# Kernel optimization log

Measured on AMD Instinct MI355X. Metric: run time of the kernel, lower is better.

The kernel has to match this reference:

```python
import jax, jax.numpy as jnp
import numpy as np

B, F, V, C = 2048, 2048, 50257, 50257


def setup_inputs() -> dict:
    key = jax.random.key(0)
    ks = jax.random.split(key, 16)
    s = 0.02  # init scale
    return {
        "X": jax.random.randint(ks[0], (B,), 0, V),
        "h": jax.random.normal(ks[1], (B, F), jnp.float32),
        "c": jax.random.normal(ks[2], (B, F), jnp.float32),
        "emb": jax.random.normal(ks[3], (V, F), jnp.float32) * s,
        "Wf": jax.random.normal(ks[4], (2 * F, F), jnp.float32) * s,
        "bf": jnp.zeros((F,), jnp.float32),
        "Wi": jax.random.normal(ks[5], (2 * F, F), jnp.float32) * s,
        "bi": jnp.zeros((F,), jnp.float32),
        "Wig": jax.random.normal(ks[6], (2 * F, F), jnp.float32) * s,
        "big": jnp.zeros((F,), jnp.float32),
        "Wog": jax.random.normal(ks[7], (2 * F, F), jnp.float32) * s,
        "bog": jnp.zeros((F,), jnp.float32),
        "Wcls": jax.random.normal(ks[8], (F, C), jnp.float32) * s,
        "bcls": jnp.zeros((C,), jnp.float32),
    }


def reference(X, h, c, emb, Wf, bf, Wi, bi, Wig, big, Wog, bog, Wcls, bcls):
    # Embedding lookup: [B] -> [B, F]
    x = emb[X]
    xh = jnp.concatenate([x, h], axis=-1)  # [B, 2F]
    # Fuse the four gate GEMMs into one [B,2F] @ [2F,4F] matmul.
    Wg = jnp.concatenate([Wf, Wig, Wog, Wi], axis=1)   # [2F, 4F]
    bg = jnp.concatenate([bf, big, bog, bi], axis=0)   # [4F]
    gates = xh @ Wg + bg                                # [B, 4F]
    f_pre, ig_pre, og_pre, g_pre = jnp.split(gates, 4, axis=-1)
    forget_gate = jax.nn.sigmoid(f_pre)
    input_gate = jax.nn.sigmoid(ig_pre)
    output_gate = jax.nn.sigmoid(og_pre)
    g = jnp.tanh(g_pre)
    c_new = forget_gate * c + input_gate * g
    h_new = output_gate * jnp.tanh(c_new)
    y = h_new @ Wcls + bcls  # [B, C]
    return (y, h_new, c_new)
```

## Files before the change

### kernel.cpp

```cpp
#include <hip/hip_runtime.h>
#include <hip/hip_bf16.h>

typedef __attribute__((ext_vector_type(4))) float f32x4;
typedef __attribute__((ext_vector_type(8))) short short8;
typedef __attribute__((ext_vector_type(8))) unsigned short ushort8;
typedef __attribute__((ext_vector_type(4))) unsigned short u16x4;
typedef float f4a __attribute__((ext_vector_type(4), aligned(4)));

__device__ __forceinline__ unsigned short f2bf(float f) {
  unsigned int u = __float_as_uint(f);
  u += 0x7fffu + ((u >> 16) & 1u);
  return (unsigned short)(u >> 16);
}

#define BARRIER do { asm volatile("" ::: "memory"); __builtin_amdgcn_s_barrier(); asm volatile("" ::: "memory"); } while(0)
#define LGKM0   do { asm volatile("s_waitcnt lgkmcnt(0)" ::: "memory"); __builtin_amdgcn_sched_barrier(0); } while(0)
#define VMW(n)  asm volatile("s_waitcnt vmcnt(" #n ")" ::: "memory")

__global__ __launch_bounds__(256) void k_build_xh(
    const int* __restrict__ X, const float* __restrict__ h,
    const float* __restrict__ emb, unsigned short* __restrict__ xh) {
  int b = blockIdx.x;
  int tid = threadIdx.x;
  int j0 = tid * 16;
  const float* src;
  if (j0 < 2048) {
    int xb = X[b];
    src = emb + (size_t)xb * 2048 + j0;
  } else {
    src = h + (size_t)b * 2048 + (j0 - 2048);
  }
  unsigned short* dst = xh + (size_t)b * 4096 + j0;
#pragma unroll
  for (int half = 0; half < 2; ++half) {
    float4 f0 = *(const float4*)(src + half * 8);
    float4 f1 = *(const float4*)(src + half * 8 + 4);
    ushort8 o;
    o[0] = f2bf(f0.x); o[1] = f2bf(f0.y); o[2] = f2bf(f0.z); o[3] = f2bf(f0.w);
    o[4] = f2bf(f1.x); o[5] = f2bf(f1.y); o[6] = f2bf(f1.z); o[7] = f2bf(f1.w);
    *(ushort8*)(dst + half * 8) = o;
  }
}

__global__ __launch_bounds__(256) void k_cvt_t(
    const float* __restrict__ W, unsigned short* __restrict__ WT,
    int K, int Nin, int ldo, int rowoff) {
  int tid = threadIdx.x;
  int lane = tid & 63, w = tid >> 6;
  int n0 = blockIdx.x * 64, k0 = blockIdx.y * 64;
  int nb = n0 + 4 * (lane & 15);
  int kb = k0 + w * 16 + 4 * (lane >> 4);
  float v[4][4];
  if (nb + 3 < Nin) {
#pragma unroll
    for (int r = 0; r < 4; ++r) {
      f4a x = *(const f4a*)(W + (size_t)(kb + r) * Nin + nb);
      v[r][0] = x.x; v[r][1] = x.y; v[r][2] = x.z; v[r][3] = x.w;
    }
  } else {
#pragma unroll
    for (int r = 0; r < 4; ++r)
#pragma unroll
      for (int e = 0; e < 4; ++e)
        v[r][e] = (nb + e < Nin) ? W[(size_t)(kb + r) * Nin + nb + e] : 0.f;
  }
#pragma unroll
  for (int e = 0; e < 4; ++e) {
    if (nb + e < Nin) {
      u16x4 o;
      o[0] = f2bf(v[0][e]); o[1] = f2bf(v[1][e]);
      o[2] = f2bf(v[2][e]); o[3] = f2bf(v[3][e]);
      *(u16x4*)(WT + (size_t)(rowoff + nb + e) * ldo + kb) = o;
    }
  }
}

__device__ __forceinline__ void stage_unit(
    const unsigned short* __restrict__ gp0, int ld, int row0, int rowmax,
    int ktile, unsigned char* smem, unsigned lds_off, int tid, int wid) {
#pragma unroll
  for (int i = 0; i < 2; ++i) {
    unsigned phys = (unsigned)(i * 512 + tid) * 16u;
    unsigned logi = phys ^ (((phys >> 7) & 7u) << 4);
    int r = (int)(logi >> 7);
    int kb = (int)(logi & 127u);
    int grow = row0 + r;
    grow = (grow > rowmax) ? rowmax : grow;
    const unsigned short* gp = gp0 + (size_t)grow * ld + ktile * 64 + (kb >> 1);
    __builtin_amdgcn_global_load_lds(
        (const __attribute__((address_space(1))) void*)gp,
        (__attribute__((address_space(3))) void*)(smem + lds_off + (unsigned)(i * 512 + wid * 64) * 16u),
        16, 0, 0);
  }
}

__device__ __forceinline__ short8 ld_fragA(const unsigned char* smem, int buf, int half,
                                           int row_local, int ks, int lane) {
  unsigned kbyte = (unsigned)(ks * 64 + ((lane >> 4) << 4));
  unsigned off = (unsigned)(buf * 2 + half) * 16384u + (unsigned)row_local * 128u
               + (kbyte ^ (((unsigned)row_local & 7u) << 4));
  return *(const short8*)(smem + off);
}
__device__ __forceinline__ short8 ld_fragB(const unsigned char* smem, int buf, int half,
                                           int col_local, int ks, int lane) {
  unsigned kbyte = (unsigned)(ks * 64 + ((lane >> 4) << 4));
  unsigned off = 65536u + (unsigned)(buf * 2 + half) * 16384u + (unsigned)col_local * 128u
               + (kbyte ^ (((unsigned)col_local & 7u) << 4));
  return *(const short8*)(smem + off);
}

__global__ __launch_bounds__(512, 1) void k_gemm256(
    const unsigned short* __restrict__ A, const unsigned short* __restrict__ Bt,
    const float* __restrict__ bias, float* __restrict__ C,
    int N, int K, int lda, int ldb, int rowmaxB) {
  __shared__ __align__(16) unsigned char smem[131072];
  const int tid = threadIdx.x, lane = tid & 63, wid = tid >> 6;
  const int wr = wid >> 2, wc = wid & 3;

  int nwg = gridDim.x * gridDim.y;
  int o = blockIdx.y * gridDim.x + blockIdx.x;
  int q = nwg >> 3;
  int s = (o & 7) * q + (o >> 3);
  const int mrow0 = (s & 7) * 256;
  const int ncol0 = (s >> 3) * 256;

  const int NKT = K >> 6;

  f32x4 acc[8][4];
#pragma unroll
  for (int m = 0; m < 8; ++m)
#pragma unroll
    for (int n = 0; n < 4; ++n) acc[m][n] = {0.f, 0.f, 0.f, 0.f};

  short8 a_frag[4][2], b_frag[2][2][2];

#define ST_A(buf, h, t) stage_unit(A, lda, mrow0 + (h) * 128, 0x7fffffff, (t), smem, (unsigned)((buf) * 2 + (h)) * 16384u, tid, wid)
#define ST_B(buf, h, t) stage_unit(Bt, ldb, ncol0 + (h) * 128, rowmaxB, (t), smem, 65536u + (unsigned)((buf) * 2 + (h)) * 16384u, tid, wid)
#define RD_A(buf, mh) do { _Pragma("unroll") for (int mm = 0; mm < 4; ++mm) { int rl = (mh) * 64 + mm * 16 + (lane & 15); _Pragma("unroll") for (int ks = 0; ks < 2; ++ks) a_frag[mm][ks] = ld_fragA(smem, (buf), wr, rl, ks, lane); } } while (0)
#define RD_B(buf, nh) do { _Pragma("unroll") for (int nn = 0; nn < 2; ++nn) { int cl = (wc & 1) * 64 + (nh) * 32 + nn * 16 + (lane & 15); _Pragma("unroll") for (int ks = 0; ks < 2; ++ks) b_frag[nh][nn][ks] = ld_fragB(smem, (buf), (wc >> 1), cl, ks, lane); } } while (0)
#define MF(mh, nh) do { __builtin_amdgcn_s_setprio(1); _Pragma("unroll") for (int mm = 0; mm < 4; ++mm) _Pragma("unroll") for (int nn = 0; nn < 2; ++nn) _Pragma("unroll") for (int ks = 0; ks < 2; ++ks) acc[(mh) * 4 + mm][(nh) * 2 + nn] = __builtin_amdgcn_mfma_f32_16x16x32_bf16(a_frag[mm][ks], b_frag[(nh)][nn][ks], acc[(mh) * 4 + mm][(nh) * 2 + nn], 0, 0, 0); __builtin_amdgcn_s_setprio(0); } while (0)

  ST_A(0, 0, 0); ST_A(0, 1, 0); ST_B(0, 0, 0); ST_B(0, 1, 0);
  ST_B(1, 0, 1); ST_B(1, 1, 1);
  VMW(4); BARRIER;

  for (int t0 = 0; t0 + 3 < NKT; t0 += 2) {
    RD_A(0, 0); RD_B(0, 0); ST_A(1, 0, t0 + 1);
    BARRIER; LGKM0; MF(0, 0); BARRIER;
    RD_B(0, 1); ST_A(1, 1, t0 + 1);
    BARRIER; LGKM0; MF(0, 1); BARRIER;
    RD_A(0, 1); ST_B(0, 0, t0 + 2);
    BARRIER; LGKM0; MF(1, 1); BARRIER;
    ST_B(0, 1, t0 + 2); VMW(4);
    BARRIER; LGKM0; MF(1, 0); BARRIER;
    RD_A(1, 0); RD_B(1, 0); ST_A(0, 0, t0 + 2);
    BARRIER; LGKM0; MF(0, 0); BARRIER;
    RD_B(1, 1); ST_A(0, 1, t0 + 2);
    BARRIER; LGKM0; MF(0, 1); BARRIER;
    RD_A(1, 1); ST_B(1, 0, t0 + 3);
    BARRIER; LGKM0; MF(1, 1); BARRIER;
    ST_B(1, 1, t0 + 3); VMW(4);
    BARRIER; LGKM0; MF(1, 0); BARRIER;
  }

  {
    const int t1 = NKT - 1;
    RD_A(0, 0); RD_B(0, 0); ST_A(1, 0, t1);
    BARRIER; LGKM0; MF(0, 0); BARRIER;
    RD_B(0, 1); ST_A(1, 1, t1);
    BARRIER; LGKM0; MF(0, 1); BARRIER;
    RD_A(0, 1);
    BARRIER; LGKM0; MF(1, 1); BARRIER;
    VMW(0);
    BARRIER; LGKM0; MF(1, 0); BARRIER;
    RD_A(1, 0); RD_B(1, 0);
    BARRIER; LGKM0; MF(0, 0); BARRIER;
    RD_B(1, 1);
    BARRIER; LGKM0; MF(0, 1); BARRIER;
    RD_A(1, 1);
    BARRIER; LGKM0; MF(1, 1); BARRIER;
    BARRIER; LGKM0; MF(1, 0); BARRIER;
  }

  {
    float* wlds = (float*)(smem + (unsigned)wid * 16384u);
    const int gcol = ncol0 + wc * 64 + lane;
    const bool cok = (gcol < N);
    const float bv = (bias != nullptr && cok) ? bias[gcol] : 0.f;
#pragma unroll
    for (int mh = 0; mh < 2; ++mh) {
#pragma unroll
      for (int mm = 0; mm < 4; ++mm)
#pragma unroll
        for (int nn = 0; nn < 4; ++nn) {
#pragma unroll
          for (int r = 0; r < 4; ++r) {
            int row = mm * 16 + ((lane >> 4) << 2) + r;
            int colv = nn * 16 + (lane & 15);
            int cs = (colv + ((row >> 2) & 3) * 16) & 63;
            wlds[row * 64 + cs] = acc[mh * 4 + mm][nn][r];
          }
        }
#pragma unroll 8
      for (int row = 0; row < 64; ++row) {
        int cs = (lane + ((row >> 2) & 3) * 16) & 63;
        float v = wlds[row * 64 + cs] + bv;
        int grow = mrow0 + wr * 128 + mh * 64 + row;
        if (cok) C[(size_t)grow * N + gcol] = v;
      }
    }
  }
#undef ST_A
#undef ST_B
#undef RD_A
#undef RD_B
#undef MF
}

__global__ __launch_bounds__(256) void k_lstm(
    const float* __restrict__ gates, const float* __restrict__ c,
    const float* __restrict__ bfp, const float* __restrict__ bigp,
    const float* __restrict__ bogp, const float* __restrict__ bip,
    float* __restrict__ hnew, float* __restrict__ cnew,
    unsigned short* __restrict__ hnew_bf) {
  int idx = blockIdx.x * 256 + threadIdx.x;
  int b = idx >> 11, j = idx & 2047;
  const float* g = gates + (size_t)b * 8192;
  float fp  = g[j]        + bfp[j];
  float igp = g[2048 + j] + bigp[j];
  float ogp = g[4096 + j] + bogp[j];
  float gp  = g[6144 + j] + bip[j];
  float f  = 1.f / (1.f + expf(-fp));
  float ig = 1.f / (1.f + expf(-igp));
  float og = 1.f / (1.f + expf(-ogp));
  float gt = tanhf(gp);
  float cn = f * c[idx] + ig * gt;
  float hn = og * tanhf(cn);
  cnew[idx] = cn;
  hnew[idx] = hn;
  hnew_bf[idx] = f2bf(hn);
}

extern "C" void kernel_launch(void* const* d_in, const int* in_sizes, int n_in,
                              void* d_out, int out_size, void* d_ws, size_t ws_size,
                              hipStream_t stream) {
  const int B = 2048, F = 2048, C = 50257;
  const int NT = 50304;
  const int*   X    = (const int*)d_in[0];
  const float* h    = (const float*)d_in[1];
  const float* c    = (const float*)d_in[2];
  const float* emb  = (const float*)d_in[3];
  const float* Wf   = (const float*)d_in[4];
  const float* bf   = (const float*)d_in[5];
  const float* Wi   = (const float*)d_in[6];
  const float* bi   = (const float*)d_in[7];
  const float* Wig  = (const float*)d_in[8];
  const float* big  = (const float*)d_in[9];
  const float* Wog  = (const float*)d_in[10];
  const float* bog  = (const float*)d_in[11];
  const float* Wcls = (const float*)d_in[12];
  const float* bcls = (const float*)d_in[13];

  float* y    = (float*)d_out;
  float* hnew = y + (size_t)B * C;
  float* cnew = hnew + (size_t)B * F;

  char* ws = (char*)d_ws;
  unsigned short* hnbf  = (unsigned short*)ws;
  unsigned short* xh    = (unsigned short*)(ws + 8388608);
  unsigned short* WgT   = (unsigned short*)(ws + 25165824);
  float*          gates = (float*)(ws + 92274688);
  unsigned short* WclsT = (unsigned short*)(ws + 8388608);

  k_build_xh<<<B, 256, 0, stream>>>(X, h, emb, xh);

  const float* parts[4] = {Wf, Wig, Wog, Wi};
  for (int p = 0; p < 4; ++p)
    k_cvt_t<<<dim3(32, 64), 256, 0, stream>>>(parts[p], WgT, 4096, 2048, 4096, p * 2048);

  k_gemm256<<<dim3(8, 32), 512, 0, stream>>>(xh, WgT, nullptr, gates, 8192, 4096, 4096, 4096, 8191);

  k_lstm<<<(B * F) / 256, 256, 0, stream>>>(gates, c, bf, big, bog, bi,
                                            hnew, cnew, hnbf);

  k_cvt_t<<<dim3(786, 32), 256, 0, stream>>>(Wcls, WclsT, 2048, C, 2048, 0);

  k_gemm256<<<dim3(8, 197), 512, 0, stream>>>(hnbf, WclsT, bcls, y, C, 2048, 2048, 2048, NT - 1);
}
```

Measured before the change: 790.1 us.

## Fuse LSTM cell into gate GEMM epilogue, interleave gate weights, add classifier tail kernel

Gate weights are now transposed in a single launch and interleaved per 64-column group, so each 256-column gate GEMM tile holds all four gates for the same 64 hidden units. The LSTM nonlinearity and state update then run in the GEMM epilogue through LDS, which removes the fp32 gates buffer round trip and the separate k_lstm kernel. The classifier GEMM now covers 192 full 256-wide column tiles, and a new 128x128 tail kernel handles the remaining ~1100 columns so fewer clamped, wasted columns are computed. Staging addresses are precomputed once per kernel instead of recomputed each stage, and the sched_barrier after lgkmcnt waits is dropped, which may change instruction scheduling. The extra __syncthreads in the fused epilogue and the small, unpipelined tail kernel add some cost in exchange.

```diff
diff --git a/kernel.cpp b/kernel.cpp
--- a/kernel.cpp
+++ b/kernel.cpp
@@ -14,7 +14,7 @@
 }
 
 #define BARRIER do { asm volatile("" ::: "memory"); __builtin_amdgcn_s_barrier(); asm volatile("" ::: "memory"); } while(0)
-#define LGKM0   do { asm volatile("s_waitcnt lgkmcnt(0)" ::: "memory"); __builtin_amdgcn_sched_barrier(0); } while(0)
+#define LGKM    asm volatile("s_waitcnt lgkmcnt(0)" ::: "memory")
 #define VMW(n)  asm volatile("s_waitcnt vmcnt(" #n ")" ::: "memory")
 
 __global__ __launch_bounds__(256) void k_build_xh(
@@ -42,9 +42,36 @@
   }
 }
 
+__global__ __launch_bounds__(256) void k_cvt_wg(
+    const float* __restrict__ W0, const float* __restrict__ W1,
+    const float* __restrict__ W2, const float* __restrict__ W3,
+    unsigned short* __restrict__ WT) {
+  const int g = blockIdx.z;
+  const float* W = (g == 0) ? W0 : (g == 1) ? W1 : (g == 2) ? W2 : W3;
+  int tid = threadIdx.x, lane = tid & 63, w = tid >> 6;
+  int n0 = blockIdx.x * 64, k0 = blockIdx.y * 64;
+  int nb = n0 + 4 * (lane & 15);
+  int kb = k0 + w * 16 + 4 * (lane >> 4);
+  float v[4][4];
+#pragma unroll
+  for (int r = 0; r < 4; ++r) {
+    f4a x = *(const f4a*)(W + (size_t)(kb + r) * 2048 + nb);
+    v[r][0] = x.x; v[r][1] = x.y; v[r][2] = x.z; v[r][3] = x.w;
+  }
+#pragma unroll
+  for (int e = 0; e < 4; ++e) {
+    int col = nb + e;
+    int row = ((col >> 6) << 8) + g * 64 + (col & 63);
+    u16x4 o;
+    o[0] = f2bf(v[0][e]); o[1] = f2bf(v[1][e]);
+    o[2] = f2bf(v[2][e]); o[3] = f2bf(v[3][e]);
+    *(u16x4*)(WT + (size_t)row * 4096 + kb) = o;
+  }
+}
+
 __global__ __launch_bounds__(256) void k_cvt_t(
     const float* __restrict__ W, unsigned short* __restrict__ WT,
-    int K, int Nin, int ldo, int rowoff) {
+    int K, int Nin, int ldo) {
   int tid = threadIdx.x;
   int lane = tid & 63, w = tid >> 6;
   int n0 = blockIdx.x * 64, k0 = blockIdx.y * 64;
@@ -70,29 +97,16 @@
       u16x4 o;
       o[0] = f2bf(v[0][e]); o[1] = f2bf(v[1][e]);
       o[2] = f2bf(v[2][e]); o[3] = f2bf(v[3][e]);
-      *(u16x4*)(WT + (size_t)(rowoff + nb + e) * ldo + kb) = o;
-    }
-  }
-}
-
-__device__ __forceinline__ void stage_unit(
-    const unsigned short* __restrict__ gp0, int ld, int row0, int rowmax,
-    int ktile, unsigned char* smem, unsigned lds_off, int tid, int wid) {
-#pragma unroll
-  for (int i = 0; i < 2; ++i) {
-    unsigned phys = (unsigned)(i * 512 + tid) * 16u;
-    unsigned logi = phys ^ (((phys >> 7) & 7u) << 4);
-    int r = (int)(logi >> 7);
-    int kb = (int)(logi & 127u);
-    int grow = row0 + r;
-    grow = (grow > rowmax) ? rowmax : grow;
-    const unsigned short* gp = gp0 + (size_t)grow * ld + ktile * 64 + (kb >> 1);
-    __builtin_amdgcn_global_load_lds(
-        (const __attribute__((address_space(1))) void*)gp,
-        (__attribute__((address_space(3))) void*)(smem + lds_off + (unsigned)(i * 512 + wid * 64) * 16u),
-        16, 0, 0);
-  }
-}
+      *(u16x4*)(WT + (size_t)(nb + e) * ldo + kb) = o;
+    }
+  }
+}
+
+struct EpiP {
+  const float *c, *b0, *b1, *b2, *b3;
+  float *hnew, *cnew;
+  unsigned short* hnbf;
+};
 
 __device__ __forceinline__ short8 ld_fragA(const unsigned char* smem, int buf, int half,
                                            int row_local, int ks, int lane) {
@@ -109,10 +123,11 @@
   return *(const short8*)(smem + off);
 }
 
+template <int EPI>
 __global__ __launch_bounds__(512, 1) void k_gemm256(
     const unsigned short* __restrict__ A, const unsigned short* __restrict__ Bt,
     const float* __restrict__ bias, float* __restrict__ C,
-    int N, int K, int lda, int ldb, int rowmaxB) {
+    int N, int K, int lda, int ldb, int rowmaxB, EpiP P) {
   __shared__ __align__(16) unsigned char smem[131072];
   const int tid = threadIdx.x, lane = tid & 63, wid = tid >> 6;
   const int wr = wid >> 2, wc = wid & 3;
@@ -126,6 +141,24 @@
 
   const int NKT = K >> 6;
 
+  unsigned vA[2], vB[2][2];
+#pragma unroll
+  for (int i = 0; i < 2; ++i) {
+    unsigned phys = (unsigned)(i * 512 + tid) * 16u;
+    unsigned logi = phys ^ (((phys >> 7) & 7u) << 4);
+    unsigned r = logi >> 7;
+    unsigned kbe = (logi & 127u) >> 1;
+    vA[i] = r * (unsigned)lda + kbe;
+#pragma unroll
+    for (int hh = 0; hh < 2; ++hh) {
+      int br = ncol0 + hh * 128 + (int)r;
+      br = (br > rowmaxB) ? rowmaxB : br;
+      vB[hh][i] = (unsigned)br * (unsigned)ldb + kbe;
+    }
+  }
+  const unsigned short* Ab0 = A + (size_t)mrow0 * lda;
+  const unsigned short* Ab1 = Ab0 + (size_t)128 * lda;
+
   f32x4 acc[8][4];
 #pragma unroll
   for (int m = 0; m < 8; ++m)
@@ -134,8 +167,15 @@
 
   short8 a_frag[4][2], b_frag[2][2][2];
 
-#define ST_A(buf, h, t) stage_unit(A, lda, mrow0 + (h) * 128, 0x7fffffff, (t), smem, (unsigned)((buf) * 2 + (h)) * 16384u, tid, wid)
-#define ST_B(buf, h, t) stage_unit(Bt, ldb, ncol0 + (h) * 128, rowmaxB, (t), smem, 65536u + (unsigned)((buf) * 2 + (h)) * 16384u, tid, wid)
+#define STG(baseptr, v, ldsoff) __builtin_amdgcn_global_load_lds( \
+    (const __attribute__((address_space(1))) void*)((baseptr) + (v)), \
+    (__attribute__((address_space(3))) void*)(smem + (ldsoff)), 16, 0, 0)
+#define ST_A(buf, hh, t) do { const unsigned short* _b = (hh ? Ab1 : Ab0) + (size_t)(t) * 64; \
+    STG(_b, vA[0], (unsigned)((buf) * 2 + (hh)) * 16384u + (unsigned)(wid * 1024)); \
+    STG(_b, vA[1], (unsigned)((buf) * 2 + (hh)) * 16384u + (unsigned)(8192 + wid * 1024)); } while (0)
+#define ST_B(buf, hh, t) do { const unsigned short* _b = Bt + (size_t)(t) * 64; \
+    STG(_b, vB[hh][0], 65536u + (unsigned)((buf) * 2 + (hh)) * 16384u + (unsigned)(wid * 1024)); \
+    STG(_b, vB[hh][1], 65536u + (unsigned)((buf) * 2 + (hh)) * 16384u + (unsigned)(8192 + wid * 1024)); } while (0)
 #define RD_A(buf, mh) do { _Pragma("unroll") for (int mm = 0; mm < 4; ++mm) { int rl = (mh) * 64 + mm * 16 + (lane & 15); _Pragma("unroll") for (int ks = 0; ks < 2; ++ks) a_frag[mm][ks] = ld_fragA(smem, (buf), wr, rl, ks, lane); } } while (0)
 #define RD_B(buf, nh) do { _Pragma("unroll") for (int nn = 0; nn < 2; ++nn) { int cl = (wc & 1) * 64 + (nh) * 32 + nn * 16 + (lane & 15); _Pragma("unroll") for (int ks = 0; ks < 2; ++ks) b_frag[nh][nn][ks] = ld_fragB(smem, (buf), (wc >> 1), cl, ks, lane); } } while (0)
 #define MF(mh, nh) do { __builtin_amdgcn_s_setprio(1); _Pragma("unroll") for (int mm = 0; mm < 4; ++mm) _Pragma("unroll") for (int nn = 0; nn < 2; ++nn) _Pragma("unroll") for (int ks = 0; ks < 2; ++ks) acc[(mh) * 4 + mm][(nh) * 2 + nn] = __builtin_amdgcn_mfma_f32_16x16x32_bf16(a_frag[mm][ks], b_frag[(nh)][nn][ks], acc[(mh) * 4 + mm][(nh) * 2 + nn], 0, 0, 0); __builtin_amdgcn_s_setprio(0); } while (0)
@@ -146,43 +186,45 @@
 
   for (int t0 = 0; t0 + 3 < NKT; t0 += 2) {
     RD_A(0, 0); RD_B(0, 0); ST_A(1, 0, t0 + 1);
-    BARRIER; LGKM0; MF(0, 0); BARRIER;
+    BARRIER; LGKM; MF(0, 0); BARRIER;
     RD_B(0, 1); ST_A(1, 1, t0 + 1);
-    BARRIER; LGKM0; MF(0, 1); BARRIER;
+    BARRIER; LGKM; MF(0, 1); BARRIER;
     RD_A(0, 1); ST_B(0, 0, t0 + 2);
-    BARRIER; LGKM0; MF(1, 1); BARRIER;
+    BARRIER; LGKM; MF(1, 1); BARRIER;
     ST_B(0, 1, t0 + 2); VMW(4);
-    BARRIER; LGKM0; MF(1, 0); BARRIER;
+    BARRIER; LGKM; MF(1, 0); BARRIER;
     RD_A(1, 0); RD_B(1, 0); ST_A(0, 0, t0 + 2);
-    BARRIER; LGKM0; MF(0, 0); BARRIER;
+    BARRIER; LGKM; MF(0, 0); BARRIER;
     RD_B(1, 1); ST_A(0, 1, t0 + 2);
-    BARRIER; LGKM0; MF(0, 1); BARRIER;
+    BARRIER; LGKM; MF(0, 1); BARRIER;
     RD_A(1, 1); ST_B(1, 0, t0 + 3);
-    BARRIER; LGKM0; MF(1, 1); BARRIER;
+    BARRIER; LGKM; MF(1, 1); BARRIER;
     ST_B(1, 1, t0 + 3); VMW(4);
-    BARRIER; LGKM0; MF(1, 0); BARRIER;
+    BARRIER; LGKM; MF(1, 0); BARRIER;
   }
 
   {
     const int t1 = NKT - 1;
     RD_A(0, 0); RD_B(0, 0); ST_A(1, 0, t1);
-    BARRIER; LGKM0; MF(0, 0); BARRIER;
+    BARRIER; LGKM; MF(0, 0); BARRIER;
     RD_B(0, 1); ST_A(1, 1, t1);
-    BARRIER; LGKM0; MF(0, 1); BARRIER;
+    BARRIER; LGKM; MF(0, 1); BARRIER;
     RD_A(0, 1);
-    BARRIER; LGKM0; MF(1, 1); BARRIER;
+    BARRIER; LGKM; MF(1, 1); BARRIER;
     VMW(0);
-    BARRIER; LGKM0; MF(1, 0); BARRIER;
+    BARRIER; LGKM; MF(1, 0); BARRIER;
     RD_A(1, 0); RD_B(1, 0);
-    BARRIER; LGKM0; MF(0, 0); BARRIER;
+    BARRIER; LGKM; MF(0, 0); BARRIER;
     RD_B(1, 1);
-    BARRIER; LGKM0; MF(0, 1); BARRIER;
+    BARRIER; LGKM; MF(0, 1); BARRIER;
     RD_A(1, 1);
-    BARRIER; LGKM0; MF(1, 1); BARRIER;
-    BARRIER; LGKM0; MF(1, 0); BARRIER;
-  }
-
-  {
+    BARRIER; LGKM; MF(1, 1); BARRIER;
+    BARRIER; LGKM; MF(1, 0); BARRIER;
+  }
+
+  __syncthreads();
+
+  if constexpr (EPI == 0) {
     float* wlds = (float*)(smem + (unsigned)wid * 16384u);
     const int gcol = ncol0 + wc * 64 + lane;
     const bool cok = (gcol < N);
@@ -192,7 +234,7 @@
 #pragma unroll
       for (int mm = 0; mm < 4; ++mm)
 #pragma unroll
-        for (int nn = 0; nn < 4; ++nn) {
+        for (int nn = 0; nn < 4; ++nn)
 #pragma unroll
           for (int r = 0; r < 4; ++r) {
             int row = mm * 16 + ((lane >> 4) << 2) + r;
@@ -200,7 +242,6 @@
             int cs = (colv + ((row >> 2) & 3) * 16) & 63;
             wlds[row * 64 + cs] = acc[mh * 4 + mm][nn][r];
           }
-        }
 #pragma unroll 8
       for (int row = 0; row < 64; ++row) {
         int cs = (lane + ((row >> 2) & 3) * 16) & 63;
@@ -209,7 +250,51 @@
         if (cok) C[(size_t)grow * N + gcol] = v;
       }
     }
-  }
+  } else {
+    float* ep = (float*)(smem + (unsigned)wr * 65536u);
+    const int lt = (wid & 3) * 64 + lane;
+    const int jj = lt & 63;
+    const int rh = lt >> 6;
+    const int gjj = (ncol0 >> 2) + jj;
+    const float bf_ = P.b0[gjj], big_ = P.b1[gjj], bog_ = P.b2[gjj], bi_ = P.b3[gjj];
+#pragma unroll
+    for (int mh = 0; mh < 2; ++mh) {
+#pragma unroll
+      for (int mm = 0; mm < 4; ++mm)
+#pragma unroll
+        for (int nn = 0; nn < 4; ++nn)
+#pragma unroll
+          for (int r = 0; r < 4; ++r) {
+            int row = mm * 16 + ((lane >> 4) << 2) + r;
+            int colv = nn * 16 + (lane & 15);
+            int cs = (colv + ((row >> 2) & 3) * 16) & 63;
+            ep[row * 256 + wc * 64 + cs] = acc[mh * 4 + mm][nn][r];
+          }
+      __syncthreads();
+#pragma unroll
+      for (int rr = 0; rr < 16; ++rr) {
+        int row = rh * 16 + rr;
+        int rot = (jj + ((row >> 2) & 3) * 16) & 63;
+        float g0 = ep[row * 256 +   0 + rot];
+        float g1 = ep[row * 256 +  64 + rot];
+        float g2 = ep[row * 256 + 128 + rot];
+        float g3 = ep[row * 256 + 192 + rot];
+        int grow = mrow0 + wr * 128 + mh * 64 + row;
+        size_t off = (size_t)grow * 2048 + gjj;
+        float fg = 1.f / (1.f + expf(-(g0 + bf_)));
+        float ig = 1.f / (1.f + expf(-(g1 + big_)));
+        float og = 1.f / (1.f + expf(-(g2 + bog_)));
+        float gt = tanhf(g3 + bi_);
+        float cn = fg * P.c[off] + ig * gt;
+        float hn = og * tanhf(cn);
+        P.cnew[off] = cn;
+        P.hnew[off] = hn;
+        P.hnbf[off] = f2bf(hn);
+      }
+      __syncthreads();
+    }
+  }
+#undef STG
 #undef ST_A
 #undef ST_B
 #undef RD_A
@@ -217,34 +302,91 @@
 #undef MF
 }
 
-__global__ __launch_bounds__(256) void k_lstm(
-    const float* __restrict__ gates, const float* __restrict__ c,
-    const float* __restrict__ bfp, const float* __restrict__ bigp,
-    const float* __restrict__ bogp, const float* __restrict__ bip,
-    float* __restrict__ hnew, float* __restrict__ cnew,
-    unsigned short* __restrict__ hnew_bf) {
-  int idx = blockIdx.x * 256 + threadIdx.x;
-  int b = idx >> 11, j = idx & 2047;
-  const float* g = gates + (size_t)b * 8192;
-  float fp  = g[j]        + bfp[j];
-  float igp = g[2048 + j] + bigp[j];
-  float ogp = g[4096 + j] + bogp[j];
-  float gp  = g[6144 + j] + bip[j];
-  float f  = 1.f / (1.f + expf(-fp));
-  float ig = 1.f / (1.f + expf(-igp));
-  float og = 1.f / (1.f + expf(-ogp));
-  float gt = tanhf(gp);
-  float cn = f * c[idx] + ig * gt;
-  float hn = og * tanhf(cn);
-  cnew[idx] = cn;
-  hnew[idx] = hn;
-  hnew_bf[idx] = f2bf(hn);
+__global__ __launch_bounds__(256) void k_gemm_tail(
+    const unsigned short* __restrict__ A, const unsigned short* __restrict__ Bt,
+    const float* __restrict__ bias, float* __restrict__ C,
+    int N, int K, int lda, int ncol_base) {
+  __shared__ unsigned short As[128 * 32];
+  __shared__ unsigned short Bs[128 * 32];
+  const int tid = threadIdx.x;
+  const int lane = tid & 63;
+  const int wid = tid >> 6;
+
+  int nwg = gridDim.x * gridDim.y;
+  int o = blockIdx.y * gridDim.x + blockIdx.x;
+  int q = nwg >> 3;
+  int s = (o & 7) * q + (o >> 3);
+  const int mrow0 = (s / gridDim.x) * 128;
+  const int ncol0 = ncol_base + (s % gridDim.x) * 128;
+
+  f32x4 acc[4][4];
+#pragma unroll
+  for (int m = 0; m < 4; ++m)
+#pragma unroll
+    for (int n = 0; n < 4; ++n) acc[m][n] = {0.f, 0.f, 0.f, 0.f};
+
+  const int wr = wid >> 1, wc = wid & 1;
+  const int brow0 = wr * 64, bcol0 = wc * 64;
+
+  int a_off[4], b_off[4];
+#pragma unroll
+  for (int m = 0; m < 4; ++m)
+    a_off[m] = (brow0 + m * 16 + (lane & 15)) * 32 + ((lane >> 4) << 3);
+#pragma unroll
+  for (int n = 0; n < 4; ++n)
+    b_off[n] = (bcol0 + n * 16 + (lane & 15)) * 32 + ((lane >> 4) << 3);
+
+  for (int k0 = 0; k0 < K; k0 += 32) {
+#pragma unroll
+    for (int i = 0; i < 2; ++i) {
+      int slot = i * 256 + tid;
+      int r = slot >> 2, ck = slot & 3;
+      unsigned short* la = As + (size_t)(i * 256 + wid * 64) * 8;
+      unsigned short* lb = Bs + (size_t)(i * 256 + wid * 64) * 8;
+      const unsigned short* ga = A + (size_t)(mrow0 + r) * lda + k0 + ck * 8;
+      const unsigned short* gb = Bt + (size_t)(ncol0 + r) * K + k0 + ck * 8;
+      __builtin_amdgcn_global_load_lds(
+          (const __attribute__((address_space(1))) void*)ga,
+          (__attribute__((address_space(3))) void*)la, 16, 0, 0);
+      __builtin_amdgcn_global_load_lds(
+          (const __attribute__((address_space(1))) void*)gb,
+          (__attribute__((address_space(3))) void*)lb, 16, 0, 0);
+    }
+    __syncthreads();
+    short8 af[4], bfr[4];
+#pragma unroll
+    for (int m = 0; m < 4; ++m) af[m] = *(const short8*)&As[a_off[m]];
+#pragma unroll
+    for (int n = 0; n < 4; ++n) bfr[n] = *(const short8*)&Bs[b_off[n]];
+#pragma unroll
+    for (int m = 0; m < 4; ++m)
+#pragma unroll
+      for (int n = 0; n < 4; ++n)
+        acc[m][n] = __builtin_amdgcn_mfma_f32_16x16x32_bf16(af[m], bfr[n], acc[m][n], 0, 0, 0);
+    __syncthreads();
+  }
+
+#pragma unroll
+  for (int n = 0; n < 4; ++n) {
+    int col = ncol0 + bcol0 + n * 16 + (lane & 15);
+    if (col < N) {
+      float bv = bias ? bias[col] : 0.f;
+#pragma unroll
+      for (int m = 0; m < 4; ++m) {
+        int row0 = mrow0 + brow0 + m * 16 + ((lane >> 4) << 2);
+        f32x4 v = acc[m][n];
+#pragma unroll
+        for (int r = 0; r < 4; ++r)
+          C[(size_t)(row0 + r) * N + col] = v[r] + bv;
+      }
+    }
+  }
 }
 
 extern "C" void kernel_launch(void* const* d_in, const int* in_sizes, int n_in,
                               void* d_out, int out_size, void* d_ws, size_t ws_size,
                               hipStream_t stream) {
-  const int B = 2048, F = 2048, C = 50257;
+  const int B = 2048, F = 2048, Ccls = 50257;
   const int NT = 50304;
   const int*   X    = (const int*)d_in[0];
   const float* h    = (const float*)d_in[1];
@@ -262,28 +404,30 @@
   const float* bcls = (const float*)d_in[13];
 
   float* y    = (float*)d_out;
-  float* hnew = y + (size_t)B * C;
+  float* hnew = y + (size_t)B * Ccls;
   float* cnew = hnew + (size_t)B * F;
 
   char* ws = (char*)d_ws;
   unsigned short* hnbf  = (unsigned short*)ws;
   unsigned short* xh    = (unsigned short*)(ws + 8388608);
   unsigned short* WgT   = (unsigned short*)(ws + 25165824);
-  float*          gates = (float*)(ws + 92274688);
   unsigned short* WclsT = (unsigned short*)(ws + 8388608);
 
+  EpiP pz{nullptr, nullptr, nullptr, nullptr, nullptr, nullptr, nullptr, nullptr};
+
   k_build_xh<<<B, 256, 0, stream>>>(X, h, emb, xh);
 
-  const float* parts[4] = {Wf, Wig, Wog, Wi};
-  for (int p = 0; p < 4; ++p)
-    k_cvt_t<<<dim3(32, 64), 256, 0, stream>>>(parts[p], WgT, 4096, 2048, 4096, p * 2048);
-
-  k_gemm256<<<dim3(8, 32), 512, 0, stream>>>(xh, WgT, nullptr, gates, 8192, 4096, 4096, 4096, 8191);
-
-  k_lstm<<<(B * F) / 256, 256, 0, stream>>>(gates, c, bf, big, bog, bi,
-                                            hnew, cnew, hnbf);
-
-  k_cvt_t<<<dim3(786, 32), 256, 0, stream>>>(Wcls, WclsT, 2048, C, 2048, 0);
-
-  k_gemm256<<<dim3(8, 197), 512, 0, stream>>>(hnbf, WclsT, bcls, y, C, 2048, 2048, 2048, NT - 1);
-}
+  k_cvt_wg<<<dim3(32, 64, 4), 256, 0, stream>>>(Wf, Wig, Wog, Wi, WgT);
+
+  EpiP pl{c, bf, big, bog, bi, hnew, cnew, hnbf};
+  k_gemm256<1><<<dim3(8, 32), 512, 0, stream>>>(
+      xh, WgT, nullptr, nullptr, 8192, 4096, 4096, 4096, 8191, pl);
+
+  k_cvt_t<<<dim3(786, 32), 256, 0, stream>>>(Wcls, WclsT, 2048, Ccls, 2048);
+
+  k_gemm256<0><<<dim3(8, 192), 512, 0, stream>>>(
+      hnbf, WclsT, bcls, y, Ccls, 2048, 2048, 2048, NT - 1, pz);
+
+  k_gemm_tail<<<dim3(9, 16), 256, 0, stream>>>(
+      hnbf, WclsT, bcls, y, Ccls, 2048, 2048, 49152);
+}
```

After: 783.6 us. Within noise of the previous version (-0.8%).
